# Optimization experiments

Hardware: AMD Instinct MI355X
Metric: run time of the kernel (lower is better)

## Reference

```python
import jax, jax.numpy as jnp
import numpy as np

B, L, D, H = 16, 3072, 512, 8
DH = D // H
TOP_K = int(5 * np.log(L))  # = 40, matches int(top_k_factor * np.log(L))


def setup_inputs() -> dict:
    key = jax.random.key(0)
    ks = jax.random.split(key, 11)
    s = 1.0 / np.sqrt(D)
    return {
        "query": jax.random.normal(ks[0], (B, L, D), jnp.float32),
        "key": jax.random.normal(ks[1], (B, L, D), jnp.float32),
        "value": jax.random.normal(ks[2], (B, L, D), jnp.float32),
        "Wq": jax.random.normal(ks[3], (D, D), jnp.float32) * s,
        "bq": jnp.zeros((D,), jnp.float32),
        "Wk": jax.random.normal(ks[4], (D, D), jnp.float32) * s,
        "bk": jnp.zeros((D,), jnp.float32),
        "Wv": jax.random.normal(ks[5], (D, D), jnp.float32) * s,
        "bv": jnp.zeros((D,), jnp.float32),
        "Wo": jax.random.normal(ks[6], (D, D), jnp.float32) * s,
        "bo": jnp.zeros((D,), jnp.float32),
    }


def reference(query, key, value, Wq, bq, Wk, bk, Wv, bv, Wo, bo):
    # projections (torch Linear: x @ W.T + b), reshape to [B, L, H, DH]
    Q = (query @ Wq.T + bq).reshape(B, L, H, DH)
    K = (key @ Wk.T + bk).reshape(B, L, H, DH)
    V = (value @ Wv.T + bv).reshape(B, L, H, DH)

    # FFT-based autocorrelation along the time axis (axis=1), same as
    # torch's rfft over last axis after permuting to [B,H,DH,L].
    q_fft = jnp.fft.rfft(Q, n=L, axis=1)
    k_fft = jnp.fft.rfft(K, n=L, axis=1)
    autocorr = jnp.fft.irfft(q_fft * jnp.conj(k_fft), n=L, axis=1)  # [B, L, H, DH]

    # top-k over the lag dimension (axis=1)
    ac_t = jnp.transpose(autocorr, (0, 2, 3, 1))  # [B, H, DH, L]
    top_vals, top_idx = jax.lax.top_k(ac_t, TOP_K)  # [B, H, DH, K]
    top_vals = jnp.transpose(top_vals, (0, 3, 1, 2))  # [B, K, H, DH]
    top_idx = jnp.transpose(top_idx, (0, 3, 1, 2))    # [B, K, H, DH]
    weights = jax.nn.softmax(top_vals, axis=1)         # softmax over k dim

    # per-k mean delay, truncated to int (matches .mean().int().item())
    shifts = jnp.mean(top_idx.astype(jnp.float32), axis=(0, 2, 3)).astype(jnp.int32)  # [K]

    w_k = jnp.transpose(weights, (1, 0, 2, 3))  # [K, B, H, DH]

    def step(agg, inp):
        shift, w = inp  # scalar int, [B, H, DH]
        rolled = jnp.roll(V, -shift, axis=1)      # [B, L, H, DH]
        return agg + rolled * w[:, None, :, :], None

    agg0 = jnp.zeros_like(Q)
    agg, _ = jax.lax.scan(step, agg0, (shifts, w_k))

    out = agg.reshape(B, L, D) @ Wo.T + bo
    return out
```

## Files before the change

### kernel.cpp

```cpp
#include <hip/hip_runtime.h>
#include <hip/hip_bf16.h>
#include <math.h>

#define B_ 16
#define L_ 3072
#define D_ 512
#define CH_ (B_ * D_)
#define TOPK_ 40
#define NCAND_ 64
#define CFLOOR_ 52
#define RFN_ 24

typedef unsigned short ushort_t;
typedef unsigned int uint_t;
typedef __attribute__((ext_vector_type(8))) short bh8;
typedef __attribute__((ext_vector_type(4))) float f4;
typedef __attribute__((ext_vector_type(4))) int i4;

__device__ __forceinline__ uint_t cvt_pk_bf16(float a, float b) {
  uint_t r;
  asm("v_cvt_pk_bf16_f32 %0, %1, %2" : "=v"(r) : "v"(a), "v"(b));
  return r;
}

__device__ __forceinline__ int swzq(int b) { return b ^ (((b >> 7) & 3) << 4); }
__device__ __forceinline__ int swzk(int b) { return b ^ (((b >> 9) & 7) << 4); }

template <int NPASS, int BK, int ST>
__device__ __forceinline__ void stage_rows(const float* __restrict__ g0,
                                           ushort_t* __restrict__ Hh,
                                           ushort_t* __restrict__ Hm,
                                           ushort_t* __restrict__ Hl,
                                           int tid) {
  const int row = tid >> 1;
  const int cb = (tid & 1) * (BK / 2);
  const float* g = g0 + (size_t)row * 512 + cb;
  ushort_t* ph = Hh + row * ST + cb;
  ushort_t* pm = Hm + row * ST + cb;
  ushort_t* pl = Hl + row * ST + cb;
#pragma unroll
  for (int p = 0; p < BK / 8; ++p) {
    float4 v = *(const float4*)(g + 4 * p);
    uint_t h01 = cvt_pk_bf16(v.x, v.y);
    uint_t h23 = cvt_pk_bf16(v.z, v.w);
    *(uint2*)(ph + 4 * p) = make_uint2(h01, h23);
    if (NPASS >= 3) {
      float x0 = __builtin_bit_cast(float, h01 << 16);
      float x1 = __builtin_bit_cast(float, h01 & 0xFFFF0000u);
      float x2 = __builtin_bit_cast(float, h23 << 16);
      float x3 = __builtin_bit_cast(float, h23 & 0xFFFF0000u);
      float r0 = v.x - x0, r1 = v.y - x1, r2 = v.z - x2, r3 = v.w - x3;
      uint_t m01 = cvt_pk_bf16(r0, r1);
      uint_t m23 = cvt_pk_bf16(r2, r3);
      if (NPASS == 3) {
        *(uint2*)(pl + 4 * p) = make_uint2(m01, m23);
      } else {
        *(uint2*)(pm + 4 * p) = make_uint2(m01, m23);
        float y0 = __builtin_bit_cast(float, m01 << 16);
        float y1 = __builtin_bit_cast(float, m01 & 0xFFFF0000u);
        float y2 = __builtin_bit_cast(float, m23 << 16);
        float y3 = __builtin_bit_cast(float, m23 & 0xFFFF0000u);
        uint_t l01 = cvt_pk_bf16(r0 - y0, r1 - y1);
        uint_t l23 = cvt_pk_bf16(r2 - y2, r3 - y3);
        *(uint2*)(pl + 4 * p) = make_uint2(l01, l23);
      }
    }
  }
}

template <int NPASS, bool ATR, bool BIAS_N>
__global__ __launch_bounds__(256) void gemm_mfma(const float* __restrict__ Ap,
                                                 const float* __restrict__ Bp,
                                                 const float* __restrict__ bias,
                                                 float* __restrict__ Cp,
                                                 long aBS, long bBS, long cBS,
                                                 int cld) {
  constexpr int BK = (NPASS == 1) ? 64 : 32;
  constexpr int ST = (NPASS == 1) ? 72 : 40;
  __shared__ ushort_t Ah[128 * ST];
  __shared__ ushort_t Bh[128 * ST];
  __shared__ ushort_t Al[(NPASS >= 3) ? 128 * ST : 8];
  __shared__ ushort_t Bl[(NPASS >= 3) ? 128 * ST : 8];
  __shared__ ushort_t Am[(NPASS == 6) ? 128 * ST : 8];
  __shared__ ushort_t Bm[(NPASS == 6) ? 128 * ST : 8];

  const float* Asrc = Ap + (size_t)blockIdx.z * aBS;
  const float* Bsrc = Bp + (size_t)blockIdx.z * bBS;
  float* Cb = Cp + (size_t)blockIdx.z * cBS;
  const int n0 = blockIdx.x * 128, m0 = blockIdx.y * 128;
  const int tid = threadIdx.x;
  const int lane = tid & 63, w = tid >> 6;
  const int wr = w >> 1, wc = w & 1;
  const int lj = lane & 15, lg = lane >> 4;

  f4 acc[4][4];
#pragma unroll
  for (int fm = 0; fm < 4; ++fm)
#pragma unroll
    for (int fn = 0; fn < 4; ++fn) acc[fm][fn] = (f4){0.f, 0.f, 0.f, 0.f};

  for (int kc = 0; kc < 512; kc += BK) {
    if (!ATR) {
      stage_rows<NPASS, BK, ST>(Asrc + (size_t)m0 * 512 + kc, Ah, Am, Al, tid);
    } else {
      constexpr int TPC = 256 / BK;
      constexpr int TC  = 128 / TPC;
      const int jl = tid / TPC, ts = tid % TPC;
      const float* g = Asrc + (size_t)(kc + jl) * L_ + m0 + ts * TC;
#pragma unroll
      for (int p = 0; p < TC / 4; ++p) {
        float4 v = *(const float4*)(g + 4 * p);
        uint_t h01 = cvt_pk_bf16(v.x, v.y);
        uint_t h23 = cvt_pk_bf16(v.z, v.w);
        int t = ts * TC + 4 * p;
        Ah[(t + 0) * ST + jl] = (ushort_t)(h01 & 0xFFFFu);
        Ah[(t + 1) * ST + jl] = (ushort_t)(h01 >> 16);
        Ah[(t + 2) * ST + jl] = (ushort_t)(h23 & 0xFFFFu);
        Ah[(t + 3) * ST + jl] = (ushort_t)(h23 >> 16);
      }
    }
    stage_rows<NPASS, BK, ST>(Bsrc + (size_t)n0 * 512 + kc, Bh, Bm, Bl, tid);
    __syncthreads();

#pragma unroll
    for (int ks = 0; ks < BK / 32; ++ks) {
      const int kk = ks * 32 + 8 * lg;
      bh8 af[4], bf[4];
#pragma unroll
      for (int f = 0; f < 4; ++f)
        af[f] = *(const bh8*)&Ah[(64 * wr + 16 * f + lj) * ST + kk];
#pragma unroll
      for (int f = 0; f < 4; ++f)
        bf[f] = *(const bh8*)&Bh[(64 * wc + 16 * f + lj) * ST + kk];
#pragma unroll
      for (int fm = 0; fm < 4; ++fm)
#pragma unroll
        for (int fn = 0; fn < 4; ++fn)
          acc[fm][fn] = __builtin_amdgcn_mfma_f32_16x16x32_bf16(af[fm], bf[fn],
                                                                acc[fm][fn], 0, 0, 0);
      if (NPASS >= 3) {
        bh8 bl_[4];
#pragma unroll
        for (int f = 0; f < 4; ++f)
          bl_[f] = *(const bh8*)&Bl[(64 * wc + 16 * f + lj) * ST + kk];
        bh8 al_[4];
#pragma unroll
        for (int f = 0; f < 4; ++f)
          al_[f] = *(const bh8*)&Al[(64 * wr + 16 * f + lj) * ST + kk];
        if (NPASS == 3) {
#pragma unroll
          for (int fm = 0; fm < 4; ++fm)
#pragma unroll
            for (int fn = 0; fn < 4; ++fn)
              acc[fm][fn] = __builtin_amdgcn_mfma_f32_16x16x32_bf16(af[fm], bl_[fn],
                                                                    acc[fm][fn], 0, 0, 0);
#pragma unroll
          for (int fm = 0; fm < 4; ++fm)
#pragma unroll
            for (int fn = 0; fn < 4; ++fn)
              acc[fm][fn] = __builtin_amdgcn_mfma_f32_16x16x32_bf16(al_[fm], bf[fn],
                                                                    acc[fm][fn], 0, 0, 0);
        } else {
          bh8 am_[4], bm_[4];
#pragma unroll
          for (int f = 0; f < 4; ++f)
            am_[f] = *(const bh8*)&Am[(64 * wr + 16 * f + lj) * ST + kk];
#pragma unroll
          for (int f = 0; f < 4; ++f)
            bm_[f] = *(const bh8*)&Bm[(64 * wc + 16 * f + lj) * ST + kk];
#pragma unroll
          for (int fm = 0; fm < 4; ++fm)
#pragma unroll
            for (int fn = 0; fn < 4; ++fn)
              acc[fm][fn] = __builtin_amdgcn_mfma_f32_16x16x32_bf16(af[fm], bm_[fn],
                                                                    acc[fm][fn], 0, 0, 0);
#pragma unroll
          for (int fm = 0; fm < 4; ++fm)
#pragma unroll
            for (int fn = 0; fn < 4; ++fn)
              acc[fm][fn] = __builtin_amdgcn_mfma_f32_16x16x32_bf16(am_[fm], bf[fn],
                                                                    acc[fm][fn], 0, 0, 0);
#pragma unroll
          for (int fm = 0; fm < 4; ++fm)
#pragma unroll
            for (int fn = 0; fn < 4; ++fn)
              acc[fm][fn] = __builtin_amdgcn_mfma_f32_16x16x32_bf16(am_[fm], bm_[fn],
                                                                    acc[fm][fn], 0, 0, 0);
#pragma unroll
          for (int fm = 0; fm < 4; ++fm)
#pragma unroll
            for (int fn = 0; fn < 4; ++fn)
              acc[fm][fn] = __builtin_amdgcn_mfma_f32_16x16x32_bf16(af[fm], bl_[fn],
                                                                    acc[fm][fn], 0, 0, 0);
#pragma unroll
          for (int fm = 0; fm < 4; ++fm)
#pragma unroll
            for (int fn = 0; fn < 4; ++fn)
              acc[fm][fn] = __builtin_amdgcn_mfma_f32_16x16x32_bf16(al_[fm], bf[fn],
                                                                    acc[fm][fn], 0, 0, 0);
        }
      }
    }
    __syncthreads();
  }

#pragma unroll
  for (int fm = 0; fm < 4; ++fm) {
    const int mrow = m0 + 64 * wr + 16 * fm + 4 * lg;
#pragma unroll
    for (int fn = 0; fn < 4; ++fn) {
      const int ncol = n0 + 64 * wc + 16 * fn + lj;
      const float bn = BIAS_N ? bias[ncol] : 0.0f;
#pragma unroll
      for (int r = 0; r < 4; ++r) {
        float val = acc[fm][fn][r] + (BIAS_N ? bn : bias[mrow + r]);
        Cb[(size_t)(mrow + r) * cld + ncol] = val;
      }
    }
  }
}

template <int P>
__device__ __forceinline__ void ac_kloop(const char* __restrict__ qb,
                                         const char* __restrict__ kb,
                                         const int* __restrict__ aswz,
                                         int bbyte, f4 acc[4]) {
#pragma unroll
  for (int it = 0; it < 12; ++it) {
    const int t512 = it * 512;
    const int b512 = bbyte + t512;
    const int msk = ((b512 >> 9) & 7) << 4;
    const int e0 = b512 ^ msk;
    const int e1 = (b512 + 64) ^ msk;
#pragma unroll
    for (int u = 0; u < 8; ++u) {
      i4 w0 = *(const i4*)(qb + (aswz[2 * u] + t512));
      i4 w1 = *(const i4*)(qb + (aswz[2 * u + 1] + t512));
      uint_t w[8] = { (uint_t)w0.x, (uint_t)w0.y, (uint_t)w0.z, (uint_t)w0.w,
                      (uint_t)w1.x, (uint_t)w1.y, (uint_t)w1.z, (uint_t)w1.w };
      const int bb = ((u & 1) ? e1 : e0) + 128 * (u >> 1);
      bh8 Bf = *(const bh8*)(kb + bb);
#pragma unroll
      for (int e = 0; e < 4; ++e) {
        const int ro = (e >> 1) + 2 * P;
        const int sh = (e & 1) * 16;
        uint_t a0v = (uint_t)((((unsigned long long)w[ro + 1] << 32) | w[ro + 0]) >> sh);
        uint_t a1v = (uint_t)((((unsigned long long)w[ro + 2] << 32) | w[ro + 1]) >> sh);
        uint_t a2v = (uint_t)((((unsigned long long)w[ro + 3] << 32) | w[ro + 2]) >> sh);
        uint_t a3v = (uint_t)((((unsigned long long)w[ro + 4] << 32) | w[ro + 3]) >> sh);
        i4 ai = { (int)a0v, (int)a1v, (int)a2v, (int)a3v };
        bh8 Af = __builtin_bit_cast(bh8, ai);
        acc[e] = __builtin_amdgcn_mfma_f32_16x16x32_bf16(Af, Bf, acc[e], 0, 0, 0);
      }
    }
  }
}

__global__ __launch_bounds__(256) void cand_refine_kernel(const float* __restrict__ Q,
                                                          const float* __restrict__ K,
                                                          double* __restrict__ top_vals,
                                                          int* __restrict__ top_idx,
                                                          int c0) {
  __shared__ __align__(16) char smem[24608];
  __shared__ float redf[8];
  __shared__ int   redi[4];
  __shared__ int   cnt_s;
  __shared__ float cv[NCAND_];
  __shared__ int   ci[NCAND_];
  __shared__ float sv[TOPK_];
  __shared__ int   si[TOPK_];
  __shared__ double refv[RFN_];
  char* kbase = smem + 6912;
  float* ac_s = (float*)smem;
  const int c = blockIdx.x;
  const int tid = threadIdx.x;
  const float* Qp = Q + (size_t)c * L_;
  const float* Kp = K + (size_t)c * L_;

  for (int x8 = tid; x8 < 432; x8 += 256) {
    int x = x8 * 8; int src = x - (x >= L_ ? L_ : 0);
    float4 f0 = *(const float4*)(Qp + src);
    float4 f1 = *(const float4*)(Qp + src + 4);
    i4 pk = { (int)cvt_pk_bf16(f0.x, f0.y), (int)cvt_pk_bf16(f0.z, f0.w),
              (int)cvt_pk_bf16(f1.x, f1.y), (int)cvt_pk_bf16(f1.z, f1.w) };
    *(i4*)(smem + swzq(16 * x8)) = pk;
  }
  for (int x8 = tid; x8 < 736; x8 += 256) {
    int x = x8 * 8; int src = x - 2816 + (x < 2816 ? L_ : 0);
    float4 f0 = *(const float4*)(Kp + src);
    float4 f1 = *(const float4*)(Kp + src + 4);
    i4 pk = { (int)cvt_pk_bf16(f0.x, f0.y), (int)cvt_pk_bf16(f0.z, f0.w),
              (int)cvt_pk_bf16(f1.x, f1.y), (int)cvt_pk_bf16(f1.z, f1.w) };
    *(i4*)(kbase + swzk(16 * x8)) = pk;
  }
  __syncthreads();

  const int lane = tid & 63, fg = tid >> 6;
  const int lg = lane >> 4, lj = lane & 15;
  const int abyte = 16 * lg + 32 * lj + 16 * (fg >> 1);
  const int jvalid = (lj < 12) ? 1 : 0;
  const int bbyte = 5632 + 16 * lg - (jvalid ? 512 * lj : 0);

  int aswz[16];
#pragma unroll
  for (int u = 0; u < 8; ++u) {
    aswz[2 * u]     = swzq(abyte + 64 * u);
    aswz[2 * u + 1] = swzq(abyte + 64 * u + 16);
  }

  f4 acc[4];
#pragma unroll
  for (int e = 0; e < 4; ++e) acc[e] = (f4){0.f, 0.f, 0.f, 0.f};

  if (fg & 1) ac_kloop<1>(smem, kbase, aswz, bbyte, acc);
  else        ac_kloop<0>(smem, kbase, aswz, bbyte, acc);

  __syncthreads();

  if (jvalid) {
#pragma unroll
    for (int e = 0; e < 4; ++e) {
      int f = 4 * fg + e;
#pragma unroll
      for (int r = 0; r < 4; ++r) {
        int g = f + 16 * (4 * lg + r);
        ac_s[lj + 12 * g] = acc[e][r];
      }
    }
  }
  __syncthreads();

  float v[12];
#pragma unroll
  for (int it = 0; it < 12; ++it) v[it] = ac_s[tid + 256 * it];

  float lm = v[0];
#pragma unroll
  for (int it = 1; it < 12; ++it) lm = fmaxf(lm, v[it]);
  for (int o = 32; o; o >>= 1) lm = fmaxf(lm, __shfl_down(lm, o));
  if ((tid & 63) == 0) redf[tid >> 6] = lm;
  __syncthreads();
  if (tid == 0) redf[4] = fmaxf(fmaxf(redf[0], redf[1]), fmaxf(redf[2], redf[3]));
  __syncthreads();
  const float Tmax = redf[4];

  auto bcount = [&](float T) -> int {
    int lc = 0;
#pragma unroll
    for (int it = 0; it < 12; ++it) lc += (v[it] > T) ? 1 : 0;
    for (int o = 32; o; o >>= 1) lc += __shfl_down(lc, o);
    __syncthreads();
    if ((tid & 63) == 0) redi[tid >> 6] = lc;
    __syncthreads();
    return redi[0] + redi[1] + redi[2] + redi[3];
  };

  float lo = Tmax - 128.0f;
  int cl = bcount(lo);
  for (int wd = 1; wd <= 5 && cl < CFLOOR_; ++wd) {
    lo = Tmax - 128.0f * (float)(1 << wd); cl = bcount(lo);
  }
  float hi = Tmax, T = lo;
  int cT = cl;
  for (int i = 0; i < 26 && cT > NCAND_; ++i) {
    float mid = 0.5f * (lo + hi);
    int cm = bcount(mid);
    if (cm >= CFLOOR_) { lo = mid; T = mid; cT = cm; } else hi = mid;
  }

  if (tid == 0) cnt_s = 0;
  __syncthreads();
#pragma unroll
  for (int it = 0; it < 12; ++it) {
    if (v[it] > T) {
      int pos = atomicAdd(&cnt_s, 1);
      if (pos < NCAND_) {
        int m = tid + 256 * it;
        int g = m / 12, j = m - 12 * g;
        cv[pos] = v[it];
        ci[pos] = g + 256 * j;
      }
    }
  }
  __syncthreads();
  const int cnt = cnt_s < NCAND_ ? cnt_s : NCAND_;

  float* qf = (float*)smem;
  float* kf = (float*)(smem + 12304);
  if (tid >= 64) {
    for (int i = (tid - 64) * 4; i < L_; i += 768) {
      *(float4*)&qf[i] = *(const float4*)(Qp + i);
      *(float4*)&kf[i] = *(const float4*)(Kp + i);
    }
    if (tid == 64) qf[L_] = qf[0];
  } else {
    float vi = (tid < cnt) ? cv[tid] : -1e30f;
    int   ii = (tid < cnt) ? ci[tid] : (1 << 30);
    int rank = 0;
#pragma unroll 8
    for (int j = 0; j < 64; ++j) {
      float vj = __shfl(vi, j);
      int   ij = __shfl(ii, j);
      rank += ((vj > vi) || (vj == vi && ij < ii)) ? 1 : 0;
    }
    if (rank < TOPK_) { sv[rank] = vi; si[rank] = (ii < L_) ? ii : 0; }
  }
  __syncthreads();

  for (int r = fg; r < RFN_; r += 4) {
    const int tau = si[r];
    double a = 0.0;
#pragma unroll 4
    for (int u = 0; u < 24; ++u) {
      int t = 2 * lane + 128 * u;
      int qi = t + tau; qi -= (qi >= L_) ? L_ : 0;
      float q0 = qf[qi], q1 = qf[qi + 1];
      float k0 = kf[t],  k1 = kf[t + 1];
      a = fma((double)q0, (double)k0, a);
      a = fma((double)q1, (double)k1, a);
    }
#pragma unroll
    for (int o = 32; o; o >>= 1) a += __shfl_down(a, o);
    if (lane == 0) refv[r] = a;
  }
  __syncthreads();

  double* out_v = top_vals + (size_t)(c0 + c) * TOPK_;
  int*    out_i = top_idx  + (size_t)(c0 + c) * TOPK_;
  if (tid < 64) {
    double dv = (tid < RFN_) ? refv[tid] : -1e300;
    int    di = (tid < RFN_) ? si[tid]   : (1 << 30);
    int rank = 0;
#pragma unroll 8
    for (int j = 0; j < RFN_; ++j) {
      double dj = __shfl(dv, j);
      int    ij = __shfl(di, j);
      rank += ((dj > dv) || (dj == dv && ij < di)) ? 1 : 0;
    }
    if (tid < RFN_) { out_v[rank] = dv; out_i[rank] = di; }
    if (tid >= RFN_ && tid < TOPK_) {
      out_v[tid] = (double)sv[tid];
      out_i[tid] = si[tid];
    }
  }
}

__global__ __launch_bounds__(256) void shifts_kernel(const int* __restrict__ top_idx,
                                                     int* __restrict__ shifts) {
  const int k = blockIdx.x;
  __shared__ double sred[256];
  double s = 0.0;
  for (int c = threadIdx.x; c < CH_; c += 256) s += (double)top_idx[(size_t)c * TOPK_ + k];
  sred[threadIdx.x] = s;
  __syncthreads();
  for (int o = 128; o > 0; o >>= 1) {
    if (threadIdx.x < o) sred[threadIdx.x] += sred[threadIdx.x + o];
    __syncthreads();
  }
  if (threadIdx.x == 0) shifts[k] = (int)((float)(sred[0] / (double)CH_));
}

__global__ __launch_bounds__(256) void softmax_kernel(const double* __restrict__ top_vals,
                                                      float* __restrict__ weights) {
  const int c = blockIdx.x * 256 + threadIdx.x;
  const double* v = top_vals + (size_t)c * TOPK_;
  double m = v[0];
  for (int k = 1; k < TOPK_; ++k) m = fmax(m, v[k]);
  double sum = 0.0;
  for (int k = 0; k < TOPK_; ++k) sum += exp(v[k] - m);
  double inv = 1.0 / sum;
  for (int k = 0; k < TOPK_; ++k)
    weights[(size_t)c * TOPK_ + k] = (float)(exp(v[k] - m) * inv);
}

__global__ __launch_bounds__(256) void agg_kernel(float* __restrict__ Vc,
                                                  const float* __restrict__ weights,
                                                  const int* __restrict__ shifts) {
  const int c = blockIdx.x;
  __shared__ float v_s[L_ + 4];
  __shared__ float w_s[TOPK_];
  __shared__ int   s_s[TOPK_];
  float* row = Vc + (size_t)c * L_;
  for (int i = threadIdx.x * 4; i < L_; i += 1024)
    *(float4*)&v_s[i] = *(const float4*)(row + i);
  if (threadIdx.x < TOPK_) {
    w_s[threadIdx.x] = weights[(size_t)c * TOPK_ + threadIdx.x];
    s_s[threadIdx.x] = shifts[threadIdx.x];
  }
  __syncthreads();
  if (threadIdx.x < 4) v_s[L_ + threadIdx.x] = v_s[threadIdx.x];
  __syncthreads();
  for (int t = threadIdx.x * 4; t < L_; t += 1024) {
    float s0 = 0.f, s1 = 0.f, s2 = 0.f, s3 = 0.f;
#pragma unroll
    for (int k = 0; k < TOPK_; ++k) {
      int idx = t + s_s[k];
      if (idx >= L_) idx -= L_;
      const float w = w_s[k];
      s0 = fmaf(w, v_s[idx],     s0);
      s1 = fmaf(w, v_s[idx + 1], s1);
      s2 = fmaf(w, v_s[idx + 2], s2);
      s3 = fmaf(w, v_s[idx + 3], s3);
    }
    float4 o = { s0, s1, s2, s3 };
    *(float4*)(row + t) = o;
  }
}

extern "C" void kernel_launch(void* const* d_in, const int* in_sizes, int n_in,
                              void* d_out, int out_size, void* d_ws, size_t ws_size,
                              hipStream_t stream) {
  const float* query = (const float*)d_in[0];
  const float* key   = (const float*)d_in[1];
  const float* value = (const float*)d_in[2];
  const float* Wq = (const float*)d_in[3];
  const float* bq = (const float*)d_in[4];
  const float* Wk = (const float*)d_in[5];
  const float* bk = (const float*)d_in[6];
  const float* Wv = (const float*)d_in[7];
  const float* bvp = (const float*)d_in[8];
  const float* Wo = (const float*)d_in[9];
  const float* bo = (const float*)d_in[10];
  float* out = (float*)d_out;
  char* ws = (char*)d_ws;

  auto al = [](size_t x) { return (x + 255) & ~(size_t)255; };
  size_t off = 0;
  const size_t tv_off = off; off = al(off + (size_t)CH_ * TOPK_ * 8);
  const size_t ti_off = off; off = al(off + (size_t)CH_ * TOPK_ * 4);
  const size_t w_off  = off; off = al(off + (size_t)CH_ * TOPK_ * 4);
  const size_t sh_off = off; off = al(off + (size_t)TOPK_ * 4);
  const size_t small_end = off;

  const size_t QK1   = (size_t)D_ * L_ * 4;
  const size_t PBQK  = al(2 * QK1);
  const size_t AGG_BYTES    = (size_t)CH_ * L_ * 4;
  const size_t BOUNCE_BYTES = (size_t)D_ * L_ * 4;

  int nb; bool bounce;
  if (ws_size >= small_end + AGG_BYTES + PBQK) {
    bounce = false;
    size_t n = (ws_size - small_end - AGG_BYTES) / PBQK;
    nb = (int)(n > 16 ? 16 : n);
  } else {
    bounce = true;
    size_t rem = (ws_size > small_end + BOUNCE_BYTES) ? (ws_size - small_end - BOUNCE_BYTES) : 0;
    size_t n = rem / PBQK; nb = (int)(n > 16 ? 16 : n);
    if (nb < 1) nb = 1;
  }

  double* top_vals = (double*)(ws + tv_off);
  int*    top_idx  = (int*)(ws + ti_off);
  float*  weights  = (float*)(ws + w_off);
  int*    shifts   = (int*)(ws + sh_off);

  float* VcAgg;
  float* bounce_buf = nullptr;
  size_t qk_off;
  if (!bounce) {
    VcAgg = (float*)(ws + small_end);
    qk_off = small_end + al(AGG_BYTES);
  } else {
    bounce_buf = (float*)(ws + small_end);
    qk_off = small_end + al(BOUNCE_BYTES);
    VcAgg = (float*)d_out;
  }
  float* Qc = (float*)(ws + qk_off);
  float* Kc = (float*)(ws + qk_off + al((size_t)nb * QK1));

  dim3 blk(256);
  const long bXS = (long)L_ * D_;
  const long cQS = (long)D_ * L_;

  for (int b0 = 0; b0 < B_; b0 += nb) {
    int nbb = (B_ - b0 < nb) ? (B_ - b0) : nb;
    dim3 gp(L_ / 128, D_ / 128, nbb);
    gemm_mfma<6, false, false><<<gp, blk, 0, stream>>>(
        Wq, query + (size_t)b0 * L_ * D_, bq, Qc, 0, bXS, cQS, L_);
    gemm_mfma<6, false, false><<<gp, blk, 0, stream>>>(
        Wk, key + (size_t)b0 * L_ * D_, bk, Kc, 0, bXS, cQS, L_);
    cand_refine_kernel<<<nbb * D_, blk, 0, stream>>>(Qc, Kc, top_vals, top_idx, b0 * D_);
  }
  shifts_kernel<<<TOPK_, blk, 0, stream>>>(top_idx, shifts);
  softmax_kernel<<<CH_ / 256, blk, 0, stream>>>(top_vals, weights);

  {
    dim3 gp(L_ / 128, D_ / 128, B_);
    gemm_mfma<1, false, false><<<gp, blk, 0, stream>>>(
        Wv, value, bvp, VcAgg, 0, bXS, cQS, L_);
  }
  agg_kernel<<<CH_, blk, 0, stream>>>(VcAgg, weights, shifts);

  if (!bounce) {
    dim3 go(D_ / 128, L_ / 128, B_);
    gemm_mfma<1, true, true><<<go, blk, 0, stream>>>(
        VcAgg, Wo, bo, out, cQS, 0, bXS, D_);
  } else {
    for (int b = 0; b < B_; ++b) {
      hipMemcpyAsync(bounce_buf, VcAgg + (size_t)b * D_ * L_, BOUNCE_BYTES,
                     hipMemcpyDeviceToDevice, stream);
      dim3 go(D_ / 128, L_ / 128, 1);
      gemm_mfma<1, true, true><<<go, blk, 0, stream>>>(
          bounce_buf, Wo, bo, out + (size_t)b * L_ * D_, 0, 0, 0, D_);
    }
  }
  (void)in_sizes; (void)n_in; (void)out_size;
}
```

Before: 1.077 ms.

## Merge Q/K projection GEMMs into one launch and split autocorr k-loop across waves

The Q and K projection GEMMs are fused into a single kernel launch that picks weights and inputs by grid z, which removes one launch and lets the two GEMMs share one larger grid. In the candidate kernel, each wave now computes 8 output fragments over half of the lag/time range instead of 4 fragments over the full range. The two halves are summed in shared memory with an extra barrier. This reuses each loaded A-word across more MFMAs, at the cost of more accumulator registers and an extra sync plus read-modify-write pass.

```diff
diff --git a/kernel.cpp b/kernel.cpp
--- a/kernel.cpp
+++ b/kernel.cpp
@@ -69,25 +69,16 @@
 }
 
 template <int NPASS, bool ATR, bool BIAS_N>
-__global__ __launch_bounds__(256) void gemm_mfma(const float* __restrict__ Ap,
-                                                 const float* __restrict__ Bp,
-                                                 const float* __restrict__ bias,
-                                                 float* __restrict__ Cp,
-                                                 long aBS, long bBS, long cBS,
-                                                 int cld) {
+__device__ __forceinline__ void gemm_core(const float* __restrict__ Asrc,
+                                          const float* __restrict__ Bsrc,
+                                          const float* __restrict__ bias,
+                                          float* __restrict__ Cb,
+                                          int n0, int m0, int cld,
+                                          ushort_t* Ah, ushort_t* Bh,
+                                          ushort_t* Am, ushort_t* Bm,
+                                          ushort_t* Al, ushort_t* Bl) {
   constexpr int BK = (NPASS == 1) ? 64 : 32;
   constexpr int ST = (NPASS == 1) ? 72 : 40;
-  __shared__ ushort_t Ah[128 * ST];
-  __shared__ ushort_t Bh[128 * ST];
-  __shared__ ushort_t Al[(NPASS >= 3) ? 128 * ST : 8];
-  __shared__ ushort_t Bl[(NPASS >= 3) ? 128 * ST : 8];
-  __shared__ ushort_t Am[(NPASS == 6) ? 128 * ST : 8];
-  __shared__ ushort_t Bm[(NPASS == 6) ? 128 * ST : 8];
-
-  const float* Asrc = Ap + (size_t)blockIdx.z * aBS;
-  const float* Bsrc = Bp + (size_t)blockIdx.z * bBS;
-  float* Cb = Cp + (size_t)blockIdx.z * cBS;
-  const int n0 = blockIdx.x * 128, m0 = blockIdx.y * 128;
   const int tid = threadIdx.x;
   const int lane = tid & 63, w = tid >> 6;
   const int wr = w >> 1, wc = w & 1;
@@ -220,14 +211,61 @@
   }
 }
 
-template <int P>
-__device__ __forceinline__ void ac_kloop(const char* __restrict__ qb,
-                                         const char* __restrict__ kb,
-                                         const int* __restrict__ aswz,
-                                         int bbyte, f4 acc[4]) {
-#pragma unroll
-  for (int it = 0; it < 12; ++it) {
-    const int t512 = it * 512;
+template <int NPASS, bool ATR, bool BIAS_N>
+__global__ __launch_bounds__(256) void gemm_mfma(const float* __restrict__ Ap,
+                                                 const float* __restrict__ Bp,
+                                                 const float* __restrict__ bias,
+                                                 float* __restrict__ Cp,
+                                                 long aBS, long bBS, long cBS,
+                                                 int cld) {
+  constexpr int ST = (NPASS == 1) ? 72 : 40;
+  __shared__ ushort_t Ah[128 * ST];
+  __shared__ ushort_t Bh[128 * ST];
+  __shared__ ushort_t Al[(NPASS >= 3) ? 128 * ST : 8];
+  __shared__ ushort_t Bl[(NPASS >= 3) ? 128 * ST : 8];
+  __shared__ ushort_t Am[(NPASS == 6) ? 128 * ST : 8];
+  __shared__ ushort_t Bm[(NPASS == 6) ? 128 * ST : 8];
+  gemm_core<NPASS, ATR, BIAS_N>(Ap + (size_t)blockIdx.z * aBS,
+                                Bp + (size_t)blockIdx.z * bBS, bias,
+                                Cp + (size_t)blockIdx.z * cBS,
+                                blockIdx.x * 128, blockIdx.y * 128, cld,
+                                Ah, Bh, Am, Bm, Al, Bl);
+}
+
+__global__ __launch_bounds__(256) void gemm6_qk(const float* __restrict__ Xq,
+                                                const float* __restrict__ Xk,
+                                                const float* __restrict__ Wq_,
+                                                const float* __restrict__ Wk_,
+                                                const float* __restrict__ bq_,
+                                                const float* __restrict__ bk_,
+                                                float* __restrict__ Pq,
+                                                float* __restrict__ Pk,
+                                                int nbb) {
+  __shared__ ushort_t Ah[128 * 40];
+  __shared__ ushort_t Bh[128 * 40];
+  __shared__ ushort_t Al[128 * 40];
+  __shared__ ushort_t Bl[128 * 40];
+  __shared__ ushort_t Am[128 * 40];
+  __shared__ ushort_t Bm[128 * 40];
+  const int z = blockIdx.z;
+  const bool isK = (z >= nbb);
+  const int b = isK ? (z - nbb) : z;
+  const float* Asrc = isK ? Wk_ : Wq_;
+  const float* Bsrc = (isK ? Xk : Xq) + (size_t)b * L_ * D_;
+  const float* bias = isK ? bk_ : bq_;
+  float* Cb = (isK ? Pk : Pq) + (size_t)b * D_ * L_;
+  gemm_core<6, false, false>(Asrc, Bsrc, bias, Cb,
+                             blockIdx.x * 128, blockIdx.y * 128, L_,
+                             Ah, Bh, Am, Bm, Al, Bl);
+}
+
+__device__ __forceinline__ void ac_kloop8(const char* __restrict__ qb,
+                                          const char* __restrict__ kb,
+                                          const int* __restrict__ aswz,
+                                          int bbyte, int tbase, f4 acc[8]) {
+#pragma unroll
+  for (int it = 0; it < 6; ++it) {
+    const int t512 = tbase + it * 512;
     const int b512 = bbyte + t512;
     const int msk = ((b512 >> 9) & 7) << 4;
     const int e0 = b512 ^ msk;
@@ -241,8 +279,8 @@
       const int bb = ((u & 1) ? e1 : e0) + 128 * (u >> 1);
       bh8 Bf = *(const bh8*)(kb + bb);
 #pragma unroll
-      for (int e = 0; e < 4; ++e) {
-        const int ro = (e >> 1) + 2 * P;
+      for (int e = 0; e < 8; ++e) {
+        const int ro = e >> 1;
         const int sh = (e & 1) * 16;
         uint_t a0v = (uint_t)((((unsigned long long)w[ro + 1] << 32) | w[ro + 0]) >> sh);
         uint_t a1v = (uint_t)((((unsigned long long)w[ro + 2] << 32) | w[ro + 1]) >> sh);
@@ -297,9 +335,12 @@
 
   const int lane = tid & 63, fg = tid >> 6;
   const int lg = lane >> 4, lj = lane & 15;
-  const int abyte = 16 * lg + 32 * lj + 16 * (fg >> 1);
+  const int fh = fg & 1;
+  const int th = fg >> 1;
+  const int abyte = 16 * lg + 32 * lj + 16 * fh;
   const int jvalid = (lj < 12) ? 1 : 0;
   const int bbyte = 5632 + 16 * lg - (jvalid ? 512 * lj : 0);
+  const int tbase = th * 3072;
 
   int aswz[16];
 #pragma unroll
@@ -308,23 +349,34 @@
     aswz[2 * u + 1] = swzq(abyte + 64 * u + 16);
   }
 
-  f4 acc[4];
-#pragma unroll
-  for (int e = 0; e < 4; ++e) acc[e] = (f4){0.f, 0.f, 0.f, 0.f};
-
-  if (fg & 1) ac_kloop<1>(smem, kbase, aswz, bbyte, acc);
-  else        ac_kloop<0>(smem, kbase, aswz, bbyte, acc);
-
-  __syncthreads();
-
-  if (jvalid) {
-#pragma unroll
-    for (int e = 0; e < 4; ++e) {
-      int f = 4 * fg + e;
+  f4 acc[8];
+#pragma unroll
+  for (int e = 0; e < 8; ++e) acc[e] = (f4){0.f, 0.f, 0.f, 0.f};
+
+  ac_kloop8(smem, kbase, aswz, bbyte, tbase, acc);
+
+  __syncthreads();
+
+  if (th == 0 && jvalid) {
+#pragma unroll
+    for (int e = 0; e < 8; ++e) {
+      int f = 8 * fh + e;
 #pragma unroll
       for (int r = 0; r < 4; ++r) {
         int g = f + 16 * (4 * lg + r);
         ac_s[lj + 12 * g] = acc[e][r];
+      }
+    }
+  }
+  __syncthreads();
+  if (th == 1 && jvalid) {
+#pragma unroll
+    for (int e = 0; e < 8; ++e) {
+      int f = 8 * fh + e;
+#pragma unroll
+      for (int r = 0; r < 4; ++r) {
+        int g = f + 16 * (4 * lg + r);
+        ac_s[lj + 12 * g] += acc[e][r];
       }
     }
   }
@@ -574,11 +626,10 @@
 
   for (int b0 = 0; b0 < B_; b0 += nb) {
     int nbb = (B_ - b0 < nb) ? (B_ - b0) : nb;
-    dim3 gp(L_ / 128, D_ / 128, nbb);
-    gemm_mfma<6, false, false><<<gp, blk, 0, stream>>>(
-        Wq, query + (size_t)b0 * L_ * D_, bq, Qc, 0, bXS, cQS, L_);
-    gemm_mfma<6, false, false><<<gp, blk, 0, stream>>>(
-        Wk, key + (size_t)b0 * L_ * D_, bk, Kc, 0, bXS, cQS, L_);
+    dim3 gp(L_ / 128, D_ / 128, 2 * nbb);
+    gemm6_qk<<<gp, blk, 0, stream>>>(query + (size_t)b0 * L_ * D_,
+                                     key   + (size_t)b0 * L_ * D_,
+                                     Wq, Wk, bq, bk, Qc, Kc, nbb);
     cand_refine_kernel<<<nbb * D_, blk, 0, stream>>>(Qc, Kc, top_vals, top_idx, b0 * D_);
   }
   shifts_kernel<<<TOPK_, blk, 0, stream>>>(top_idx, shifts);
```

Result: faster. 1.054 ms (-2.1%).
